# Kernel tuning notes

Measured on AMD Instinct MI355X. Metric: run time of the kernel, lower is better.

## Reference

```python
import jax, jax.numpy as jnp
import numpy as np

DMIN, DMAX = -1.0, 1.0
B, I, O, K = 1024, 256, 256, 128

def setup_inputs() -> dict:
    key = jax.random.key(0)
    k1, k2, k3 = jax.random.split(key, 3)
    x = jax.random.normal(k1, (B, I), dtype=jnp.float32)
    bound = 1.0 / np.sqrt(I)
    base_weight = jax.random.uniform(k2, (O, I), dtype=jnp.float32, minval=-bound, maxval=bound)
    coeff = 0.03 * jax.random.normal(k3, (O, I, K), dtype=jnp.float32)
    coeff = coeff - coeff.mean(axis=-1, keepdims=True)
    return {
        'x': x,
        'base_weight': base_weight,
        'spline_coefficients': coeff,
        'spline_scale': jnp.ones((O, I), dtype=jnp.float32),
        'bias': jnp.zeros((O,), dtype=jnp.float32),
    }


def reference(x, base_weight, spline_coefficients, spline_scale, bias):
    num_knots = spline_coefficients.shape[-1]
    step = (DMAX - DMIN) / (num_knots - 1)
    # input activation (tanh) then clamp to spline domain
    p = jnp.tanh(x)                                   # (B, I)
    c = jnp.clip(p, DMIN, DMAX)
    scaled = (c - DMIN) / step                        # in [0, K-1]
    left = jnp.clip(jnp.floor(scaled).astype(jnp.int32), 0, num_knots - 1)
    right = jnp.minimum(left + 1, num_knots - 1)
    frac = scaled - left.astype(p.dtype)              # (B, I)
    # fold spline_scale into coefficients, then gather only the 2 relevant knots
    Cs = spline_coefficients * spline_scale[..., None]  # (O, I, K)
    ii = jnp.arange(x.shape[1])[None, :]                # (1, I) broadcasts with (B, I)
    cl = Cs[:, ii, left]                                # (O, B, I)
    cr = Cs[:, ii, right]                               # (O, B, I)
    spline = jnp.einsum('bi,obi->bo', 1.0 - frac, cl) + jnp.einsum('bi,obi->bo', frac, cr)
    base = jax.nn.silu(p) @ base_weight.T               # (B, O)
    return base + spline + bias[None, :]
```

## Files before the change

### kernel.cpp

```cpp
#include <hip/hip_runtime.h>

constexpr int Bb = 1024;
constexpr int Ii = 256;
constexpr int Oo = 256;
constexpr int Kk = 128;
constexpr int NCH = 8;

typedef unsigned short u16;
typedef u16 ushort4v __attribute__((ext_vector_type(4)));

__device__ __forceinline__ float bf16u_to_f(u16 u) {
    union { unsigned int ui; float f; } c;
    c.ui = ((unsigned int)u) << 16;
    return c.f;
}
__device__ __forceinline__ u16 f_to_bf16(float f) {
    union { float f; unsigned int u; } c; c.f = f;
    unsigned int r = c.u + 0x7fffu + ((c.u >> 16) & 1u);
    return (u16)(r >> 16);
}

__global__ void kprep(const float* __restrict__ x, const float* __restrict__ wbase,
                      float4* __restrict__ fls, float* __restrict__ wt) {
    int tid = blockIdx.x * 256 + threadIdx.x;
    float xv = x[tid];
    float e2 = __expf(2.f * xv);
    float p = 1.f - 2.f / (e2 + 1.f);
    float s = p / (1.f + __expf(-p));
    float c = fminf(fmaxf(p, -1.f), 1.f);
    float scaled = (c + 1.f) * ((float)(Kk - 1) * 0.5f);
    int l = (int)floorf(scaled);
    l = min(max(l, 0), Kk - 1);
    int r = min(l + 1, Kk - 1);
    float f = scaled - (float)l;
    float4 v;
    v.x = f;
    v.y = s;
    v.z = __int_as_float(l * (Oo * 2));
    v.w = __int_as_float(r * (Oo * 2));
    fls[tid] = v;

    if (tid < Ii * Oo) wt[tid] = wbase[(tid & 255) * Ii + (tid >> 8)];
}

__global__ __launch_bounds__(256) void kperm(const float* __restrict__ cs,
                                             const float* __restrict__ scale,
                                             u16* __restrict__ cp) {
    __shared__ u16 T[128 * 130];
    int i  = blockIdx.x >> 1;
    int o0 = (blockIdx.x & 1) << 7;
    int t = threadIdx.x;

    {
        int c4 = t & 31;
        int rb = t >> 5;
        const float4* cs4 = (const float4*)cs;
#pragma unroll
        for (int p = 0; p < 16; ++p) {
            int r = p * 8 + rb;
            int o = o0 + r;
            float sc = scale[o * Ii + i];
            float4 val = cs4[(size_t)(o * Ii + i) * (Kk / 4) + c4];
            unsigned int lo = ((unsigned int)f_to_bf16(val.y * sc) << 16) | f_to_bf16(val.x * sc);
            unsigned int hi = ((unsigned int)f_to_bf16(val.w * sc) << 16) | f_to_bf16(val.z * sc);
            *(unsigned int*)&T[r * 130 + c4 * 4]     = lo;
            *(unsigned int*)&T[r * 130 + c4 * 4 + 2] = hi;
        }
    }
    __syncthreads();
    {
        int ol = t & 127;
        int kh = t >> 7;
        u16* dst = cp + ((size_t)i * Kk) * Oo + o0 + ol;
#pragma unroll
        for (int p = 0; p < 64; ++p) {
            int k = p * 2 + kh;
            dst[(size_t)k * Oo] = T[ol * 130 + k];
        }
    }
}

__global__ __launch_bounds__(256, 4) void kmain(const float4* __restrict__ fls,
                                                const char* __restrict__ cpb,
                                                const float4* __restrict__ wt4,
                                                float4* __restrict__ part4) {
    __shared__ float4 sf[128];
    int t = threadIdx.x;
    int blk = blockIdx.x;
    int chunk = blk & (NCH - 1);
    int b0 = (blk >> 3) << 2;
    int i0 = chunk << 5;

    if (t < 128) {
        int il = t >> 2, bl = t & 3;
        sf[t] = fls[(size_t)(b0 + bl) * Ii + i0 + il];
    }
    __syncthreads();

    int oq = t & 63;
    int bh = t >> 6;

    float a0 = 0.f, a1 = 0.f, a2 = 0.f, a3 = 0.f;
    const char* cbase = cpb + (size_t)i0 * (Kk * Oo * 2) + oq * 8;
#pragma unroll 8
    for (int il = 0; il < 32; ++il) {
        float4 v = sf[il * 4 + bh];
        float4 w = wt4[(i0 + il) * (Oo / 4) + oq];
        const char* ci = cbase + (size_t)il * (Kk * Oo * 2);
        ushort4v cl = *(const ushort4v*)(ci + __float_as_int(v.z));
        ushort4v cr = *(const ushort4v*)(ci + __float_as_int(v.w));
        float f = v.x, g = 1.f - v.x, s = v.y;
        a0 = fmaf(s, w.x, a0);
        a1 = fmaf(s, w.y, a1);
        a2 = fmaf(s, w.z, a2);
        a3 = fmaf(s, w.w, a3);
        a0 = fmaf(g, bf16u_to_f(cl.x), a0);
        a1 = fmaf(g, bf16u_to_f(cl.y), a1);
        a2 = fmaf(g, bf16u_to_f(cl.z), a2);
        a3 = fmaf(g, bf16u_to_f(cl.w), a3);
        a0 = fmaf(f, bf16u_to_f(cr.x), a0);
        a1 = fmaf(f, bf16u_to_f(cr.y), a1);
        a2 = fmaf(f, bf16u_to_f(cr.z), a2);
        a3 = fmaf(f, bf16u_to_f(cr.w), a3);
    }
    float4 r; r.x = a0; r.y = a1; r.z = a2; r.w = a3;
    part4[(size_t)chunk * (Bb * Oo / 4) + (size_t)(b0 + bh) * (Oo / 4) + oq] = r;
}

__global__ __launch_bounds__(256) void kreduce(const float4* __restrict__ part4,
                                               const float4* __restrict__ bias4,
                                               float4* __restrict__ out4) {
    int gid = blockIdx.x * 256 + threadIdx.x;
    const float4* p = part4 + gid;
    float4 s = p[0];
#pragma unroll
    for (int c = 1; c < NCH; ++c) {
        float4 v = p[(size_t)c * (Bb * Oo / 4)];
        s.x += v.x; s.y += v.y; s.z += v.z; s.w += v.w;
    }
    float4 bv = bias4[gid & 63];
    s.x += bv.x; s.y += bv.y; s.z += bv.z; s.w += bv.w;
    out4[gid] = s;
}

extern "C" void kernel_launch(void* const* d_in, const int* in_sizes, int n_in,
                              void* d_out, int out_size, void* d_ws, size_t ws_size,
                              hipStream_t stream) {
    const float* x     = (const float*)d_in[0];
    const float* wbase = (const float*)d_in[1];
    const float* coeff = (const float*)d_in[2];
    const float* scale = (const float*)d_in[3];
    const float* bias  = (const float*)d_in[4];
    float* out = (float*)d_out;

    char* ws = (char*)d_ws;
    float4* fls = (float4*)ws;
    size_t off = (size_t)Bb * Ii * sizeof(float4);
    u16* cp = (u16*)(ws + off);
    off += (size_t)Ii * Kk * Oo * sizeof(u16);
    float* wt = (float*)(ws + off);
    off += (size_t)Ii * Oo * sizeof(float);
    float4* part4 = (float4*)(ws + off);

    kprep<<<(Bb * Ii) / 256, 256, 0, stream>>>(x, wbase, fls, wt);
    kperm<<<Ii * 2, 256, 0, stream>>>(coeff, scale, cp);
    kmain<<<2048, 256, 0, stream>>>(fls, (const char*)cp, (const float4*)wt, part4);
    kreduce<<<(Bb * Oo / 4) / 256, 256, 0, stream>>>(part4, (const float4*)bias, (float4*)out);
}
```

Baseline: 116.8 us.

## Fuse input activation prep into main kernel and weight transpose into kperm

Removes the separate kprep launch. The tanh/silu/knot-index computation now runs inside kmain while it fills shared memory, and the base-weight transpose is folded into the tail of kperm. This drops one kernel launch and the write and re-read of the 4 MB float4 feature buffer. In exchange each activation is recomputed by every block that needs it, about 32x redundancy since each b,i pair is loaded by the 32 blocks covering different... actually by one block per chunk, adding transcendental work to kmain's prologue. The workspace layout is changed to fixed offsets.

After: 115.8 us. About the same (-0.8%).

```diff
diff --git a/kernel.cpp b/kernel.cpp
--- a/kernel.cpp
+++ b/kernel.cpp
@@ -20,32 +20,11 @@
     return (u16)(r >> 16);
 }
 
-__global__ void kprep(const float* __restrict__ x, const float* __restrict__ wbase,
-                      float4* __restrict__ fls, float* __restrict__ wt) {
-    int tid = blockIdx.x * 256 + threadIdx.x;
-    float xv = x[tid];
-    float e2 = __expf(2.f * xv);
-    float p = 1.f - 2.f / (e2 + 1.f);
-    float s = p / (1.f + __expf(-p));
-    float c = fminf(fmaxf(p, -1.f), 1.f);
-    float scaled = (c + 1.f) * ((float)(Kk - 1) * 0.5f);
-    int l = (int)floorf(scaled);
-    l = min(max(l, 0), Kk - 1);
-    int r = min(l + 1, Kk - 1);
-    float f = scaled - (float)l;
-    float4 v;
-    v.x = f;
-    v.y = s;
-    v.z = __int_as_float(l * (Oo * 2));
-    v.w = __int_as_float(r * (Oo * 2));
-    fls[tid] = v;
-
-    if (tid < Ii * Oo) wt[tid] = wbase[(tid & 255) * Ii + (tid >> 8)];
-}
-
 __global__ __launch_bounds__(256) void kperm(const float* __restrict__ cs,
                                              const float* __restrict__ scale,
-                                             u16* __restrict__ cp) {
+                                             const float* __restrict__ wbase,
+                                             u16* __restrict__ cp,
+                                             float* __restrict__ wt) {
     __shared__ u16 T[128 * 130];
     int i  = blockIdx.x >> 1;
     int o0 = (blockIdx.x & 1) << 7;
@@ -78,9 +57,13 @@
             dst[(size_t)k * Oo] = T[ol * 130 + k];
         }
     }
+    if (blockIdx.x < 256) {
+        int gid = blockIdx.x * 256 + t;
+        wt[gid] = wbase[(gid & 255) * Ii + (gid >> 8)];
+    }
 }
 
-__global__ __launch_bounds__(256, 4) void kmain(const float4* __restrict__ fls,
+__global__ __launch_bounds__(256, 4) void kmain(const float* __restrict__ x,
                                                 const char* __restrict__ cpb,
                                                 const float4* __restrict__ wt4,
                                                 float4* __restrict__ part4) {
@@ -93,7 +76,21 @@
 
     if (t < 128) {
         int il = t >> 2, bl = t & 3;
-        sf[t] = fls[(size_t)(b0 + bl) * Ii + i0 + il];
+        float xv = x[(size_t)(b0 + bl) * Ii + i0 + il];
+        float e2 = __expf(2.f * xv);
+        float p = 1.f - 2.f / (e2 + 1.f);
+        float s = p / (1.f + __expf(-p));
+        float c = fminf(fmaxf(p, -1.f), 1.f);
+        float scaled = (c + 1.f) * ((float)(Kk - 1) * 0.5f);
+        int l = (int)floorf(scaled);
+        l = min(max(l, 0), Kk - 1);
+        int rr = min(l + 1, Kk - 1);
+        float4 v;
+        v.x = scaled - (float)l;
+        v.y = s;
+        v.z = __int_as_float(l * (Oo * 2));
+        v.w = __int_as_float(rr * (Oo * 2));
+        sf[t] = v;
     }
     __syncthreads();
 
@@ -154,16 +151,11 @@
     float* out = (float*)d_out;
 
     char* ws = (char*)d_ws;
-    float4* fls = (float4*)ws;
-    size_t off = (size_t)Bb * Ii * sizeof(float4);
-    u16* cp = (u16*)(ws + off);
-    off += (size_t)Ii * Kk * Oo * sizeof(u16);
-    float* wt = (float*)(ws + off);
-    off += (size_t)Ii * Oo * sizeof(float);
-    float4* part4 = (float4*)(ws + off);
+    u16*    cp    = (u16*)ws;
+    float*  wt    = (float*)(ws + (16u << 20));
+    float4* part4 = (float4*)(ws + (17u << 20));
 
-    kprep<<<(Bb * Ii) / 256, 256, 0, stream>>>(x, wbase, fls, wt);
-    kperm<<<Ii * 2, 256, 0, stream>>>(coeff, scale, cp);
-    kmain<<<2048, 256, 0, stream>>>(fls, (const char*)cp, (const float4*)wt, part4);
+    kperm<<<Ii * 2, 256, 0, stream>>>(coeff, scale, wbase, cp, wt);
+    kmain<<<2048, 256, 0, stream>>>(x, (const char*)cp, (const float4*)wt, part4);
     kreduce<<<(Bb * Oo / 4) / 256, 256, 0, stream>>>(part4, (const float4*)bias, (float4*)out);
 }
```
